# Kernel tuning notes

Measured on AMD Instinct MI355X. Metric: run time of the kernel, lower is better.

## Reference

```python
import jax, jax.numpy as jnp
import numpy as np

ALPHA = 0.2  # LeakyReLU negative slope from init kwarg
NEG_INF = -9e15


def gat_multihead(x, adj_mask, W, a, concat):
    """Standard (GLMP-style) dense GAT, all heads at once.
    x: [B,N,Din], adj_mask: [B,N,N] bool, W: [H,Din,F], a: [H,2F].
    """
    B, N, _ = x.shape
    H, _, F = W.shape
    Wh = jnp.einsum('bnd,hdf->bhnf', x, W)              # [B,H,N,F]
    f1 = jnp.einsum('bhnf,hf->bhn', Wh, a[:, :F])
    f2 = jnp.einsum('bhnf,hf->bhn', Wh, a[:, F:])
    e = jax.nn.leaky_relu(f1[:, :, :, None] + f2[:, :, None, :], ALPHA)  # [B,H,N,N]
    e = jnp.where(adj_mask[:, None], e, NEG_INF)
    att = jax.nn.softmax(e, axis=-1)
    out = jnp.einsum('bhij,bhjf->bhif', att, Wh)        # [B,H,N,F]
    if concat:
        out = jax.nn.elu(out)
        return out.transpose(0, 2, 1, 3).reshape(B, N, H * F)
    # concat=False heads are summed and divided by nheads in load_graph -> mean
    return out.mean(axis=1)


def setup_inputs() -> dict:
    key = jax.random.key(0)
    ks = jax.random.split(key, 12)
    B, N, T = 16, 1024, 6
    V, D, F, H = 32000, 128, 64, 4
    CONV_MAX = 400
    story = jax.random.randint(ks[0], (B, N, T), 0, V)
    kb_len = jax.random.randint(ks[1], (B,), 1, CONV_MAX)
    conv_len = jax.random.randint(ks[2], (B,), 1, CONV_MAX)
    hidden = jax.random.normal(ks[3], (B, F), dtype=jnp.float32)
    dh_outputs = jax.random.normal(ks[4], (B, CONV_MAX, D), dtype=jnp.float32)
    adj = (jax.random.uniform(ks[5], (B, N, N)) < 0.05).astype(jnp.float32)
    emb = jax.random.normal(ks[6], (V, D), dtype=jnp.float32) * 0.1
    W1 = jax.random.normal(ks[7], (H, D, F), dtype=jnp.float32) * 0.1
    a1 = jax.random.normal(ks[8], (H, 2 * F), dtype=jnp.float32) * 0.1
    W2 = jax.random.normal(ks[9], (H, H * F, F), dtype=jnp.float32) * 0.1
    a2 = jax.random.normal(ks[10], (H, 2 * F), dtype=jnp.float32) * 0.1
    W3 = jax.random.normal(ks[11], (H, H * F, F), dtype=jnp.float32) * 0.1
    a3 = jax.random.normal(jax.random.fold_in(key, 99), (H, 2 * F), dtype=jnp.float32) * 0.1
    return {"story": story, "kb_len": kb_len, "conv_len": conv_len,
            "hidden": hidden, "dh_outputs": dh_outputs, "adj": adj,
            "emb": emb, "W1": W1, "a1": a1, "W2": W2, "a2": a2, "W3": W3, "a3": a3}


def reference(story, kb_len, conv_len, hidden, dh_outputs, adj, emb, W1, a1, W2, a2, W3, a3):
    B, N, T = story.shape
    Lc = dh_outputs.shape[1]
    # Embedding lookup + bag-of-words sum over memory token slots
    x = emb[story].sum(axis=2)                              # [B,N,D]
    # add_lm_embedding: scatter dh_outputs[b, :conv_len[b]] into slots
    # [kb_len[b]-1, kb_len[b]-1+conv_len[b]) of the memory (vectorized)
    pos = jnp.arange(N)[None, :]                            # [1,N]
    off = pos - (kb_len[:, None] - 1)                       # [B,N]
    valid = (off >= 0) & (off < conv_len[:, None])
    idx = jnp.clip(off, 0, Lc - 1)
    gathered = jnp.take_along_axis(dh_outputs, idx[:, :, None], axis=1)  # [B,N,D]
    x = x + jnp.where(valid[:, :, None], gathered, 0.0)
    # update_pad_token_adj: self-loop for pad slots k >= kb_len+conv_len
    d = jnp.arange(N)
    start = kb_len + conv_len                               # (kb_len-1)+conv_len+1
    diag = adj[:, d, d]
    adj = adj.at[:, d, d].set(jnp.where(d[None, :] >= start[:, None], 1.0, diag))
    adj_mask = adj > 0
    # Three GAT stacks (dropout omitted: eval mode)
    x = gat_multihead(x, adj_mask, W1, a1, concat=True)     # [B,N,H*F]
    x = gat_multihead(x, adj_mask, W2, a2, concat=True)     # [B,N,H*F]
    x = jax.nn.sigmoid(gat_multihead(x, adj_mask, W3, a3, concat=False))  # [B,N,F]
    prob_logits = jnp.einsum('bnf,bf->bn', x, hidden)       # [B,N]
    return (jax.nn.sigmoid(prob_logits), hidden, prob_logits)
```

## Files before the change

kernel.cpp:

```cpp
#include <hip/hip_runtime.h>
#include <stdint.h>

typedef short bf16x8 __attribute__((ext_vector_type(8)));
typedef float f32x4 __attribute__((ext_vector_type(4)));
typedef unsigned short u16;
typedef unsigned short u16x4 __attribute__((ext_vector_type(4)));
typedef unsigned int u32;
typedef unsigned int u32x4 __attribute__((ext_vector_type(4)));
typedef unsigned long long u64;


__device__ inline u16 f2b(float f) {
    unsigned u = __float_as_uint(f);
    u += 0x7fffu + ((u >> 16) & 1u);
    return (u16)(u >> 16);
}

__device__ inline float wred_sum(float v) {
    #pragma unroll
    for (int m = 32; m >= 1; m >>= 1) v += __shfl_xor(v, m, 64);
    return v;
}

__global__ __launch_bounds__(256) void k_pre(const float* __restrict__ adj,
                                             const int* __restrict__ kb,
                                             const int* __restrict__ cv,
                                             const int* __restrict__ story,
                                             const float* __restrict__ dh,
                                             const float* __restrict__ emb,
                                             u64* __restrict__ mask,
                                             u16* __restrict__ x0) {
    int bid = blockIdx.x;
    int tid = threadIdx.x;
    if (bid < 4096) {
        int w = tid >> 6, l = tid & 63;
        int row = bid * 4 + w;
        int b = row >> 10, i = row & 1023;
        int start = kb[b] + cv[b];
        const float* arow = adj + ((size_t)row << 10);
        u64* mrow = mask + ((size_t)row << 4);
        #pragma unroll
        for (int wd = 0; wd < 16; ++wd) {
            int j = (wd << 6) | l;
            bool p = arow[j] > 0.0f;
            if (j == i && i >= start) p = true;
            u64 bal = __ballot(p);
            if (l == 0) mrow[wd] = bal;
        }
    } else {
        int bn = ((bid - 4096) << 1) + (tid >> 7);
        int b = bn >> 10, n = bn & 1023;
        int d = tid & 127;
        const int* st = story + (size_t)bn * 6;
        float s = 0.0f;
        #pragma unroll
        for (int t = 0; t < 6; ++t) {
            int tok = st[t];
            s += emb[((size_t)tok << 7) + d];
        }
        int off = n - (kb[b] - 1);
        if (off >= 0 && off < cv[b]) s += dh[((size_t)b * 400 + off) * 128 + d];
        x0[((size_t)bn << 7) + d] = f2b(s);
    }
}

__global__ __launch_bounds__(256) void k_wa_all(const float* __restrict__ W1,
                                                const float* __restrict__ a1,
                                                const float* __restrict__ W2,
                                                const float* __restrict__ a2,
                                                const float* __restrict__ W3,
                                                const float* __restrict__ a3,
                                                float* __restrict__ wa) {
    int bid = blockIdx.x;
    const float *W, *a; float* o; int Kmask, kshift;
    if (bid < 4)       { W = W1; a = a1; o = wa;        Kmask = 127; kshift = 7; }
    else if (bid < 12) { W = W2; a = a2; o = wa + 1024; Kmask = 255; kshift = 8; bid -= 4; }
    else               { W = W3; a = a3; o = wa + 3072; Kmask = 255; kshift = 8; bid -= 12; }
    int id = bid * 256 + threadIdx.x;
    int c = id >> kshift, k = id & Kmask;
    int h = c >> 1, wh = c & 1;
    const float4* wr = (const float4*)(W + ((size_t)(h << kshift) + k) * 64);
    const float4* av = (const float4*)(a + h * 128 + wh * 64);
    float s = 0.0f;
    #pragma unroll
    for (int q = 0; q < 16; ++q) {
        float4 x = wr[q], y = av[q];
        s += x.x * y.x + x.y * y.y + x.z * y.z + x.w * y.w;
    }
    o[id] = s;
}

__global__ __launch_bounds__(256) void k_prepW_all(const float* __restrict__ W1,
                                                   const float* __restrict__ W2,
                                                   const float* __restrict__ W3,
                                                   const float* __restrict__ wa,
                                                   u16* __restrict__ Bp1,
                                                   u16* __restrict__ Bp2,
                                                   u16* __restrict__ Bp3) {
    int bid = blockIdx.x;
    const float* W; const float* wav; u16* Bp; int K;
    if (bid < 136)      { W = W1; wav = wa;        Bp = Bp1; K = 128; }
    else if (bid < 408) { W = W2; wav = wa + 1024; Bp = Bp2; K = 256; bid -= 136; }
    else                { W = W3; wav = wa + 3072; Bp = Bp3; K = 256; bid -= 408; }
    int id = bid * 256 + threadIdx.x;
    int j = id & 7, lane = (id >> 3) & 63, fr = id >> 9;
    int kt = fr / 17, ct = fr - kt * 17;
    int kk = (kt << 5) + ((lane >> 4) << 3) + j;
    u16 o;
    if (ct < 16) {
        int col = (ct << 4) | (lane & 15);
        o = f2b(W[((size_t)(col >> 6) * K + kk) * 64 + (col & 63)]);
    } else {
        int c = lane & 15;
        o = (c < 8) ? f2b(wav[c * K + kk]) : (u16)0;
    }
    Bp[id] = o;
}

template <int KT>
__global__ __launch_bounds__(256) void k_gemm(const u16* __restrict__ A,
                                              const u16* __restrict__ Bp,
                                              u16* __restrict__ WhB,
                                              float* __restrict__ f1,
                                              float* __restrict__ f2) {
    constexpr int K = KT * 32;
    __shared__ __align__(16) u16 tile[4][2048];
    int tid = threadIdx.x;
    int w = tid >> 6, l = tid & 63;
    int gw = blockIdx.x * 4 + w;
    int rt = gw >> 1, colhalf = gw & 1;
    int m0 = rt << 4;
    int b = m0 >> 10, n0 = m0 & 1023;
    int jt = n0 >> 5, halfsel = (n0 >> 4) & 1;
    const bf16x8* Av = (const bf16x8*)A;
    const bf16x8* Bv = (const bf16x8*)Bp;
    int arow = m0 + (l & 15);
    bf16x8 af[KT];
    #pragma unroll
    for (int kt = 0; kt < KT; ++kt)
        af[kt] = Av[((size_t)arow * K + (kt << 5) + ((l >> 4) << 3)) >> 3];
    f32x4 acc[8];
    #pragma unroll
    for (int c = 0; c < 8; ++c) acc[c] = f32x4{0.f, 0.f, 0.f, 0.f};
    f32x4 acc16 = {0.f, 0.f, 0.f, 0.f};
    #pragma unroll
    for (int kt = 0; kt < KT; ++kt) {
        #pragma unroll
        for (int c = 0; c < 8; ++c) {
            int ct = (colhalf << 3) + c;
            acc[c] = __builtin_amdgcn_mfma_f32_16x16x32_bf16(
                af[kt], Bv[(kt * 17 + ct) * 64 + l], acc[c], 0, 0, 0);
        }
        if (colhalf == 0)
            acc16 = __builtin_amdgcn_mfma_f32_16x16x32_bf16(
                af[kt], Bv[(kt * 17 + 16) * 64 + l], acc16, 0, 0, 0);
    }
    int co = l & 15, ro = (l >> 4) << 2;
    if (colhalf == 0 && co < 8) {
        int h = co >> 1;
        float* fp = (co & 1) ? f2 : f1;
        int base = (((b << 2) + h) << 10) + n0 + ro;
        #pragma unroll
        for (int r = 0; r < 4; ++r) fp[base + r] = acc16[r];
    }
    u16* tw = tile[w];
    #pragma unroll
    for (int c = 0; c < 8; ++c) {
        int col2 = (c << 4) + co;
        u16x4 pk;
        #pragma unroll
        for (int r = 0; r < 4; ++r) pk[r] = f2b(acc[c][r]);
        *(u16x4*)(tw + (col2 << 4) + ro) = pk;
    }
    __syncthreads();
    int lp = (halfsel << 5) + (l & 31);
    #pragma unroll
    for (int c4 = 0; c4 < 4; ++c4) {
        int combo = (c4 << 1) + (l >> 5);
        int hh = combo >> 2, ft = combo & 3;
        int col2 = (hh << 6) + (ft << 4) + (l & 15);
        int r0 = ((l >> 4) & 1) << 3;
        bf16x8 v = *(const bf16x8*)(tw + (col2 << 4) + r0);
        int h = (colhalf << 1) + hh;
        int bh = (b << 2) + h;
        size_t fidx = (size_t)((bh << 7) + (jt << 2) + ft);
        *(bf16x8*)(WhB + (fidx * 64 + lp) * 8) = v;
    }
}

#define PV_CORE(f2v4, mw, f1i, d0f, fragbase, Bv, acc, accs, g)                  \
    {                                                                            \
        u32 onep = ((l & 15) == 0) ? 0x3F803F80u : 0u;                           \
        u32x4 ov = {onep, onep, onep, onep};                                     \
        bf16x8 sfrag = __builtin_bit_cast(bf16x8, ov);                           \
        for (int jt = 0; jt < 32; ++jt) {                                        \
            u32 sh = mw[jt] >> (g << 3);                                         \
            f32x4 fa = f2v4[(jt << 3) + (g << 1)];                               \
            f32x4 fb = f2v4[(jt << 3) + (g << 1) + 1];                           \
            float p[8];                                                          \
            _Pragma("unroll")                                                    \
            for (int jj = 0; jj < 8; ++jj) {                                     \
                float f2j = (jj < 4) ? fa[jj] : fb[jj - 4];                      \
                float t = f1i + f2j;                                             \
                float e = fmaxf(t, 0.2f * t);                                    \
                float ex;                                                        \
                asm("v_exp_f32 %0, %1" : "=v"(ex) : "v"(e));                     \
                p[jj] = (sh & (1u << jj)) ? ex : d0f;                            \
            }                                                                    \
            u32x4 pk;                                                            \
            _Pragma("unroll")                                                    \
            for (int q = 0; q < 4; ++q) {                                        \
                u32 r;                                                           \
                asm("v_cvt_pk_bf16_f32 %0, %1, %2"                               \
                    : "=v"(r) : "v"(p[2 * q]), "v"(p[2 * q + 1]));               \
                pk[q] = r;                                                       \
            }                                                                    \
            bf16x8 af = __builtin_bit_cast(bf16x8, pk);                          \
            accs = __builtin_amdgcn_mfma_f32_16x16x32_bf16(af, sfrag, accs, 0, 0, 0); \
            _Pragma("unroll")                                                    \
            for (int ft = 0; ft < 4; ++ft)                                       \
                acc[ft] = __builtin_amdgcn_mfma_f32_16x16x32_bf16(               \
                    af, Bv[(size_t)(fragbase + (jt << 2) + ft) * 64 + l], acc[ft], 0, 0, 0); \
        }                                                                        \
    }

__global__ __launch_bounds__(256) void k_pv0(const u32* __restrict__ mask32,
                                             const float* __restrict__ f1g,
                                             const float* __restrict__ f2g,
                                             const bf16x8* __restrict__ Bv,
                                             u16* __restrict__ xout) {
    __shared__ __align__(16) float f2s[1024];
    const float LOG2E = 1.44269504088896340736f;
    int tid = threadIdx.x;
    int w = tid >> 6, l = tid & 63;
    int bh = blockIdx.x >> 4;
    int b = bh >> 2, h = bh & 3;
    int itile = ((blockIdx.x & 15) << 2) + w;
    int i0 = itile << 4;
    for (int idx = tid; idx < 1024; idx += 256) f2s[idx] = f2g[(bh << 10) + idx] * LOG2E;
    __syncthreads();
    int row = l & 15, g = l >> 4;
    int i = i0 + row;
    float f1i = f1g[(bh << 10) + i] * LOG2E;
    const u32x4* m4 = (const u32x4*)(mask32 + (((size_t)(b << 10) + i) << 5));
    u32 mw[32];
    #pragma unroll
    for (int t4 = 0; t4 < 8; ++t4) {
        u32x4 q = m4[t4];
        mw[t4 * 4 + 0] = q[0]; mw[t4 * 4 + 1] = q[1];
        mw[t4 * 4 + 2] = q[2]; mw[t4 * 4 + 3] = q[3];
    }
    u32 anyb = 0;
    #pragma unroll
    for (int jt = 0; jt < 32; ++jt) anyb |= mw[jt];
    float d0f = (anyb == 0u) ? 1.0f : 0.0f;
    f32x4 acc[4];
    #pragma unroll
    for (int ft = 0; ft < 4; ++ft) acc[ft] = f32x4{0.f, 0.f, 0.f, 0.f};
    f32x4 accs = {0.f, 0.f, 0.f, 0.f};
    const f32x4* f2v4 = (const f32x4*)f2s;
    int fragbase = bh << 7;
    PV_CORE(f2v4, mw, f1i, d0f, fragbase, Bv, acc, accs, g)
    #pragma unroll
    for (int reg = 0; reg < 4; ++reg) {
        int orow = (g << 2) + reg;
        float s = __shfl(accs[reg], g << 4, 64);
        float rinv = 1.0f / s;
        int grow = i0 + orow;
        #pragma unroll
        for (int ft = 0; ft < 4; ++ft) {
            float v = acc[ft][reg] * rinv;
            float e2 = v > 0.0f ? v : (__expf(v) - 1.0f);
            xout[((size_t)((b << 10) + grow) << 8) + (h << 6) + (ft << 4) + row] = f2b(e2);
        }
    }
}

__global__ __launch_bounds__(256) void k_pv3(const u32* __restrict__ mask32,
                                             const float* __restrict__ f1g,
                                             const float* __restrict__ f2g,
                                             const bf16x8* __restrict__ Bv,
                                             const float* __restrict__ hidden,
                                             float* __restrict__ dout) {
    __shared__ __align__(16) float shbuf[4096];
    const float LOG2E = 1.44269504088896340736f;
    int tid = threadIdx.x;
    int w = tid >> 6, l = tid & 63;
    int b = blockIdx.x >> 6;
    int itile = blockIdx.x & 63;
    int i0 = itile << 4;
    int bh = (b << 2) + w;
    for (int idx = tid; idx < 4096; idx += 256) shbuf[idx] = f2g[(b << 12) + idx] * LOG2E;
    __syncthreads();
    int row = l & 15, g = l >> 4;
    int i = i0 + row;
    float f1i = f1g[(bh << 10) + i] * LOG2E;
    const u32x4* m4 = (const u32x4*)(mask32 + (((size_t)(b << 10) + i) << 5));
    u32 mw[32];
    #pragma unroll
    for (int t4 = 0; t4 < 8; ++t4) {
        u32x4 q = m4[t4];
        mw[t4 * 4 + 0] = q[0]; mw[t4 * 4 + 1] = q[1];
        mw[t4 * 4 + 2] = q[2]; mw[t4 * 4 + 3] = q[3];
    }
    u32 anyb = 0;
    #pragma unroll
    for (int jt = 0; jt < 32; ++jt) anyb |= mw[jt];
    float d0f = (anyb == 0u) ? 1.0f : 0.0f;
    f32x4 acc[4];
    #pragma unroll
    for (int ft = 0; ft < 4; ++ft) acc[ft] = f32x4{0.f, 0.f, 0.f, 0.f};
    f32x4 accs = {0.f, 0.f, 0.f, 0.f};
    const f32x4* f2v4 = (const f32x4*)(shbuf + (w << 10));
    int fragbase = bh << 7;
    PV_CORE(f2v4, mw, f1i, d0f, fragbase, Bv, acc, accs, g)
    __syncthreads();
    #pragma unroll
    for (int reg = 0; reg < 4; ++reg) {
        int orow = (g << 2) + reg;
        float s = __shfl(accs[reg], g << 4, 64);
        float rinv = 1.0f / s;
        #pragma unroll
        for (int ft = 0; ft < 4; ++ft)
            shbuf[(w << 10) + (orow << 6) + (ft << 4) + row] = acc[ft][reg] * rinv;
    }
    __syncthreads();
    float hid = hidden[(b << 6) + l];
    #pragma unroll
    for (int k = 0; k < 4; ++k) {
        int rl = (k << 2) + w;
        int o = (rl << 6) + l;
        float s = shbuf[o] + shbuf[1024 + o] + shbuf[2048 + o] + shbuf[3072 + o];
        s *= 0.25f;
        float x = 1.0f / (1.0f + __expf(-s));
        float logit = wred_sum(x * hid);
        if (l == 0) {
            int grow = i0 + rl;
            dout[(b << 10) + grow] = 1.0f / (1.0f + __expf(-logit));
            dout[17408 + (b << 10) + grow] = logit;
        }
    }
    if (itile == 0 && w == 0) dout[16384 + (b << 6) + l] = hid;
}

extern "C" void kernel_launch(void* const* d_in, const int* in_sizes, int n_in,
                              void* d_out, int out_size, void* d_ws, size_t ws_size,
                              hipStream_t stream) {
    const int*   story  = (const int*)d_in[0];
    const int*   kb     = (const int*)d_in[1];
    const int*   cv     = (const int*)d_in[2];
    const float* hidden = (const float*)d_in[3];
    const float* dh     = (const float*)d_in[4];
    const float* adj    = (const float*)d_in[5];
    const float* emb    = (const float*)d_in[6];
    const float* W1     = (const float*)d_in[7];
    const float* a1     = (const float*)d_in[8];
    const float* W2     = (const float*)d_in[9];
    const float* a2     = (const float*)d_in[10];
    const float* W3     = (const float*)d_in[11];
    const float* a3     = (const float*)d_in[12];
    float* dout = (float*)d_out;

    char* ws = (char*)d_ws;
    u64*   mask   = (u64*)(ws + 0);
    u32*   mask32 = (u32*)(ws + 0);
    u16*   x0   = (u16*)(ws + 2097152);
    u16*   xbf  = (u16*)(ws + 6291456);
    u16*   WhB  = (u16*)(ws + 14680064);
    float* f1   = (float*)(ws + 23068672);
    float* f2   = (float*)(ws + 23330816);
    u16*   Bp1  = (u16*)(ws + 23592960);
    u16*   Bp2  = (u16*)(ws + 23724032);
    u16*   Bp3  = (u16*)(ws + 23863296);
    float* wa   = (float*)(ws + 24002560);

    k_wa_all<<<20, 256, 0, stream>>>(W1, a1, W2, a2, W3, a3, wa);
    k_prepW_all<<<680, 256, 0, stream>>>(W1, W2, W3, wa, Bp1, Bp2, Bp3);
    k_pre<<<12288, 256, 0, stream>>>(adj, kb, cv, story, dh, emb, mask, x0);

    k_gemm<4><<<512, 256, 0, stream>>>(x0, Bp1, WhB, f1, f2);
    k_pv0<<<1024, 256, 0, stream>>>(mask32, f1, f2, (const bf16x8*)WhB, xbf);

    k_gemm<8><<<512, 256, 0, stream>>>(xbf, Bp2, WhB, f1, f2);
    k_pv0<<<1024, 256, 0, stream>>>(mask32, f1, f2, (const bf16x8*)WhB, xbf);

    k_gemm<8><<<512, 256, 0, stream>>>(xbf, Bp3, WhB, f1, f2);
    k_pv3<<<1024, 256, 0, stream>>>(mask32, f1, f2, (const bf16x8*)WhB, hidden, dout);
}
```

Before: 163.9 us.

## Fuse weight prep into preprocessing and process two row tiles per wave

Merges the weight-projection and weight-packing kernels into the preprocessing kernel, dropping two launches. The mask builder now reads adjacency rows with vectorized loads and also precomputes a per-row empty-mask flag, and the embedding gather switches to float4 accesses. The GEMM and PV kernels each handle two 16-row tiles per wave so B fragments and f2 loads are reused across both. PV now stages mask rows in LDS, which halves the grid size but raises register pressure and lowers occupancy.

```diff
diff --git a/kernel.cpp b/kernel.cpp
--- a/kernel.cpp
+++ b/kernel.cpp
@@ -28,93 +28,102 @@
                                              const int* __restrict__ story,
                                              const float* __restrict__ dh,
                                              const float* __restrict__ emb,
+                                             const float* __restrict__ W1,
+                                             const float* __restrict__ a1,
+                                             const float* __restrict__ W2,
+                                             const float* __restrict__ a2,
+                                             const float* __restrict__ W3,
+                                             const float* __restrict__ a3,
                                              u64* __restrict__ mask,
-                                             u16* __restrict__ x0) {
+                                             u16* __restrict__ x0,
+                                             u16* __restrict__ Bp1,
+                                             u16* __restrict__ Bp2,
+                                             u16* __restrict__ Bp3,
+                                             float* __restrict__ d0g) {
     int bid = blockIdx.x;
     int tid = threadIdx.x;
-    if (bid < 4096) {
+    if (bid < 1024) {
         int w = tid >> 6, l = tid & 63;
-        int row = bid * 4 + w;
-        int b = row >> 10, i = row & 1023;
+        int rbase = (bid << 4) + (w << 2);
+        int b = rbase >> 10;
         int start = kb[b] + cv[b];
-        const float* arow = adj + ((size_t)row << 10);
-        u64* mrow = mask + ((size_t)row << 4);
-        #pragma unroll
-        for (int wd = 0; wd < 16; ++wd) {
-            int j = (wd << 6) | l;
-            bool p = arow[j] > 0.0f;
-            if (j == i && i >= start) p = true;
-            u64 bal = __ballot(p);
-            if (l == 0) mrow[wd] = bal;
-        }
-    } else {
-        int bn = ((bid - 4096) << 1) + (tid >> 7);
+        const float4* a4 = (const float4*)adj;
+        for (int r = 0; r < 4; ++r) {
+            int row = rbase + r;
+            int i = row & 1023;
+            u32 m16 = 0;
+            #pragma unroll
+            for (int q = 0; q < 4; ++q) {
+                float4 v = a4[(size_t)row * 256 + (l << 2) + q];
+                m16 |= (u32)(v.x > 0.0f) << (q * 4);
+                m16 |= (u32)(v.y > 0.0f) << (q * 4 + 1);
+                m16 |= (u32)(v.z > 0.0f) << (q * 4 + 2);
+                m16 |= (u32)(v.w > 0.0f) << (q * 4 + 3);
+            }
+            if (i >= start && (i >> 4) == l) m16 |= 1u << (i & 15);
+            u64 bal = __ballot(m16 != 0);
+            u32 s0 = (u32)__shfl((int)m16, (l << 2) + 0, 64);
+            u32 s1 = (u32)__shfl((int)m16, (l << 2) + 1, 64);
+            u32 s2 = (u32)__shfl((int)m16, (l << 2) + 2, 64);
+            u32 s3 = (u32)__shfl((int)m16, (l << 2) + 3, 64);
+            if (l < 16) {
+                u64 word = (u64)(s0 | (s1 << 16)) | ((u64)(s2 | (s3 << 16)) << 32);
+                mask[((size_t)row << 4) + l] = word;
+            }
+            if (l == 0) d0g[row] = (bal == 0ull) ? 1.0f : 0.0f;
+        }
+    } else if (bid < 3072) {
+        int w = tid >> 6, l = tid & 63;
+        int r = l >> 5, dq = l & 31;
+        int bn = ((bid - 1024) << 3) + (w << 1) + r;
         int b = bn >> 10, n = bn & 1023;
-        int d = tid & 127;
         const int* st = story + (size_t)bn * 6;
-        float s = 0.0f;
+        const float4* emb4 = (const float4*)emb;
+        float4 acc = {0.f, 0.f, 0.f, 0.f};
         #pragma unroll
         for (int t = 0; t < 6; ++t) {
             int tok = st[t];
-            s += emb[((size_t)tok << 7) + d];
+            float4 e = emb4[(size_t)tok * 32 + dq];
+            acc.x += e.x; acc.y += e.y; acc.z += e.z; acc.w += e.w;
         }
         int off = n - (kb[b] - 1);
-        if (off >= 0 && off < cv[b]) s += dh[((size_t)b * 400 + off) * 128 + d];
-        x0[((size_t)bn << 7) + d] = f2b(s);
-    }
-}
-
-__global__ __launch_bounds__(256) void k_wa_all(const float* __restrict__ W1,
-                                                const float* __restrict__ a1,
-                                                const float* __restrict__ W2,
-                                                const float* __restrict__ a2,
-                                                const float* __restrict__ W3,
-                                                const float* __restrict__ a3,
-                                                float* __restrict__ wa) {
-    int bid = blockIdx.x;
-    const float *W, *a; float* o; int Kmask, kshift;
-    if (bid < 4)       { W = W1; a = a1; o = wa;        Kmask = 127; kshift = 7; }
-    else if (bid < 12) { W = W2; a = a2; o = wa + 1024; Kmask = 255; kshift = 8; bid -= 4; }
-    else               { W = W3; a = a3; o = wa + 3072; Kmask = 255; kshift = 8; bid -= 12; }
-    int id = bid * 256 + threadIdx.x;
-    int c = id >> kshift, k = id & Kmask;
-    int h = c >> 1, wh = c & 1;
-    const float4* wr = (const float4*)(W + ((size_t)(h << kshift) + k) * 64);
-    const float4* av = (const float4*)(a + h * 128 + wh * 64);
-    float s = 0.0f;
-    #pragma unroll
-    for (int q = 0; q < 16; ++q) {
-        float4 x = wr[q], y = av[q];
-        s += x.x * y.x + x.y * y.y + x.z * y.z + x.w * y.w;
-    }
-    o[id] = s;
-}
-
-__global__ __launch_bounds__(256) void k_prepW_all(const float* __restrict__ W1,
-                                                   const float* __restrict__ W2,
-                                                   const float* __restrict__ W3,
-                                                   const float* __restrict__ wa,
-                                                   u16* __restrict__ Bp1,
-                                                   u16* __restrict__ Bp2,
-                                                   u16* __restrict__ Bp3) {
-    int bid = blockIdx.x;
-    const float* W; const float* wav; u16* Bp; int K;
-    if (bid < 136)      { W = W1; wav = wa;        Bp = Bp1; K = 128; }
-    else if (bid < 408) { W = W2; wav = wa + 1024; Bp = Bp2; K = 256; bid -= 136; }
-    else                { W = W3; wav = wa + 3072; Bp = Bp3; K = 256; bid -= 408; }
-    int id = bid * 256 + threadIdx.x;
-    int j = id & 7, lane = (id >> 3) & 63, fr = id >> 9;
-    int kt = fr / 17, ct = fr - kt * 17;
-    int kk = (kt << 5) + ((lane >> 4) << 3) + j;
-    u16 o;
-    if (ct < 16) {
-        int col = (ct << 4) | (lane & 15);
-        o = f2b(W[((size_t)(col >> 6) * K + kk) * 64 + (col & 63)]);
+        if (off >= 0 && off < cv[b]) {
+            float4 d = ((const float4*)dh)[((size_t)b * 400 + off) * 32 + dq];
+            acc.x += d.x; acc.y += d.y; acc.z += d.z; acc.w += d.w;
+        }
+        u16x4 pk = {f2b(acc.x), f2b(acc.y), f2b(acc.z), f2b(acc.w)};
+        *(u16x4*)(x0 + ((size_t)bn << 7) + (dq << 2)) = pk;
     } else {
-        int c = lane & 15;
-        o = (c < 8) ? f2b(wav[c * K + kk]) : (u16)0;
-    }
-    Bp[id] = o;
+        int pb = bid - 3072;
+        const float *W, *a; u16* Bp; int K;
+        if (pb < 136)      { W = W1; a = a1; Bp = Bp1; K = 128; }
+        else if (pb < 408) { W = W2; a = a2; Bp = Bp2; K = 256; pb -= 136; }
+        else               { W = W3; a = a3; Bp = Bp3; K = 256; pb -= 408; }
+        int id = pb * 256 + tid;
+        int j = id & 7, lane = (id >> 3) & 63, fr = id >> 9;
+        int kt = fr / 17, ct = fr - kt * 17;
+        int kk = (kt << 5) + ((lane >> 4) << 3) + j;
+        u16 o;
+        if (ct < 16) {
+            int col = (ct << 4) | (lane & 15);
+            o = f2b(W[((size_t)(col >> 6) * K + kk) * 64 + (col & 63)]);
+        } else {
+            int c = lane & 15;
+            if (c < 8) {
+                int h = c >> 1, wh = c & 1;
+                const float4* wr = (const float4*)(W + ((size_t)h * K + kk) * 64);
+                const float4* av = (const float4*)(a + h * 128 + wh * 64);
+                float s = 0.0f;
+                #pragma unroll
+                for (int q = 0; q < 16; ++q) {
+                    float4 x = wr[q], y = av[q];
+                    s += x.x * y.x + x.y * y.y + x.z * y.z + x.w * y.w;
+                }
+                o = f2b(s);
+            } else o = 0;
+        }
+        Bp[id] = o;
+    }
 }
 
 template <int KT>
@@ -124,154 +133,170 @@
                                               float* __restrict__ f1,
                                               float* __restrict__ f2) {
     constexpr int K = KT * 32;
-    __shared__ __align__(16) u16 tile[4][2048];
-    int tid = threadIdx.x;
-    int w = tid >> 6, l = tid & 63;
-    int gw = blockIdx.x * 4 + w;
-    int rt = gw >> 1, colhalf = gw & 1;
-    int m0 = rt << 4;
+    __shared__ __align__(16) u16 tile[4][2][2048];
+    int tid = threadIdx.x, w = tid >> 6, l = tid & 63;
+    int rtp = blockIdx.x;
+    int colq = w;
+    int m0 = rtp << 5;
     int b = m0 >> 10, n0 = m0 & 1023;
-    int jt = n0 >> 5, halfsel = (n0 >> 4) & 1;
+    int jt = n0 >> 5;
     const bf16x8* Av = (const bf16x8*)A;
     const bf16x8* Bv = (const bf16x8*)Bp;
-    int arow = m0 + (l & 15);
-    bf16x8 af[KT];
-    #pragma unroll
-    for (int kt = 0; kt < KT; ++kt)
-        af[kt] = Av[((size_t)arow * K + (kt << 5) + ((l >> 4) << 3)) >> 3];
-    f32x4 acc[8];
-    #pragma unroll
-    for (int c = 0; c < 8; ++c) acc[c] = f32x4{0.f, 0.f, 0.f, 0.f};
-    f32x4 acc16 = {0.f, 0.f, 0.f, 0.f};
+    int arowA = m0 + (l & 15);
+    bf16x8 afA[KT], afB[KT];
     #pragma unroll
     for (int kt = 0; kt < KT; ++kt) {
-        #pragma unroll
-        for (int c = 0; c < 8; ++c) {
-            int ct = (colhalf << 3) + c;
-            acc[c] = __builtin_amdgcn_mfma_f32_16x16x32_bf16(
-                af[kt], Bv[(kt * 17 + ct) * 64 + l], acc[c], 0, 0, 0);
-        }
-        if (colhalf == 0)
-            acc16 = __builtin_amdgcn_mfma_f32_16x16x32_bf16(
-                af[kt], Bv[(kt * 17 + 16) * 64 + l], acc16, 0, 0, 0);
+        size_t base = ((size_t)arowA * K + (kt << 5) + ((l >> 4) << 3)) >> 3;
+        afA[kt] = Av[base];
+        afB[kt] = Av[base + ((16 * K) >> 3)];
+    }
+    f32x4 accA[4], accB[4];
+    #pragma unroll
+    for (int c = 0; c < 4; ++c) { accA[c] = f32x4{0.f,0.f,0.f,0.f}; accB[c] = f32x4{0.f,0.f,0.f,0.f}; }
+    f32x4 acc16A = {0.f,0.f,0.f,0.f}, acc16B = {0.f,0.f,0.f,0.f};
+    #pragma unroll
+    for (int kt = 0; kt < KT; ++kt) {
+        #pragma unroll
+        for (int c = 0; c < 4; ++c) {
+            bf16x8 bv = Bv[(size_t)(kt * 17 + (colq << 2) + c) * 64 + l];
+            accA[c] = __builtin_amdgcn_mfma_f32_16x16x32_bf16(afA[kt], bv, accA[c], 0, 0, 0);
+            accB[c] = __builtin_amdgcn_mfma_f32_16x16x32_bf16(afB[kt], bv, accB[c], 0, 0, 0);
+        }
+        if (colq == 0) {
+            bf16x8 bv = Bv[(size_t)(kt * 17 + 16) * 64 + l];
+            acc16A = __builtin_amdgcn_mfma_f32_16x16x32_bf16(afA[kt], bv, acc16A, 0, 0, 0);
+            acc16B = __builtin_amdgcn_mfma_f32_16x16x32_bf16(afB[kt], bv, acc16B, 0, 0, 0);
+        }
     }
     int co = l & 15, ro = (l >> 4) << 2;
-    if (colhalf == 0 && co < 8) {
-        int h = co >> 1;
+    if (colq == 0 && co < 8) {
+        int hh = co >> 1;
         float* fp = (co & 1) ? f2 : f1;
-        int base = (((b << 2) + h) << 10) + n0 + ro;
-        #pragma unroll
-        for (int r = 0; r < 4; ++r) fp[base + r] = acc16[r];
-    }
-    u16* tw = tile[w];
-    #pragma unroll
-    for (int c = 0; c < 8; ++c) {
+        int base = (((b << 2) + hh) << 10) + n0 + ro;
+        #pragma unroll
+        for (int r = 0; r < 4; ++r) {
+            fp[base + r] = acc16A[r];
+            fp[base + 16 + r] = acc16B[r];
+        }
+    }
+    u16* twA = tile[w][0]; u16* twB = tile[w][1];
+    #pragma unroll
+    for (int c = 0; c < 4; ++c) {
         int col2 = (c << 4) + co;
-        u16x4 pk;
-        #pragma unroll
-        for (int r = 0; r < 4; ++r) pk[r] = f2b(acc[c][r]);
-        *(u16x4*)(tw + (col2 << 4) + ro) = pk;
+        u16x4 pkA, pkB;
+        #pragma unroll
+        for (int r = 0; r < 4; ++r) { pkA[r] = f2b(accA[c][r]); pkB[r] = f2b(accB[c][r]); }
+        *(u16x4*)(twA + (col2 << 4) + ro) = pkA;
+        *(u16x4*)(twB + (col2 << 4) + ro) = pkB;
     }
     __syncthreads();
-    int lp = (halfsel << 5) + (l & 31);
-    #pragma unroll
-    for (int c4 = 0; c4 < 4; ++c4) {
-        int combo = (c4 << 1) + (l >> 5);
-        int hh = combo >> 2, ft = combo & 3;
-        int col2 = (hh << 6) + (ft << 4) + (l & 15);
+    int bh = (b << 2) + colq;
+    int lq = l & 31;
+    #pragma unroll
+    for (int ftq = 0; ftq < 2; ++ftq) {
+        int ft = (ftq << 1) + (l >> 5);
+        int col2 = (ft << 4) + (l & 15);
         int r0 = ((l >> 4) & 1) << 3;
-        bf16x8 v = *(const bf16x8*)(tw + (col2 << 4) + r0);
-        int h = (colhalf << 1) + hh;
-        int bh = (b << 2) + h;
+        bf16x8 vA = *(const bf16x8*)(twA + (col2 << 4) + r0);
+        bf16x8 vB = *(const bf16x8*)(twB + (col2 << 4) + r0);
         size_t fidx = (size_t)((bh << 7) + (jt << 2) + ft);
-        *(bf16x8*)(WhB + (fidx * 64 + lp) * 8) = v;
-    }
-}
-
-#define PV_CORE(f2v4, mw, f1i, d0f, fragbase, Bv, acc, accs, g)                  \
-    {                                                                            \
-        u32 onep = ((l & 15) == 0) ? 0x3F803F80u : 0u;                           \
-        u32x4 ov = {onep, onep, onep, onep};                                     \
-        bf16x8 sfrag = __builtin_bit_cast(bf16x8, ov);                           \
-        for (int jt = 0; jt < 32; ++jt) {                                        \
-            u32 sh = mw[jt] >> (g << 3);                                         \
-            f32x4 fa = f2v4[(jt << 3) + (g << 1)];                               \
-            f32x4 fb = f2v4[(jt << 3) + (g << 1) + 1];                           \
-            float p[8];                                                          \
-            _Pragma("unroll")                                                    \
-            for (int jj = 0; jj < 8; ++jj) {                                     \
-                float f2j = (jj < 4) ? fa[jj] : fb[jj - 4];                      \
-                float t = f1i + f2j;                                             \
-                float e = fmaxf(t, 0.2f * t);                                    \
-                float ex;                                                        \
-                asm("v_exp_f32 %0, %1" : "=v"(ex) : "v"(e));                     \
-                p[jj] = (sh & (1u << jj)) ? ex : d0f;                            \
-            }                                                                    \
-            u32x4 pk;                                                            \
-            _Pragma("unroll")                                                    \
-            for (int q = 0; q < 4; ++q) {                                        \
-                u32 r;                                                           \
-                asm("v_cvt_pk_bf16_f32 %0, %1, %2"                               \
-                    : "=v"(r) : "v"(p[2 * q]), "v"(p[2 * q + 1]));               \
-                pk[q] = r;                                                       \
-            }                                                                    \
-            bf16x8 af = __builtin_bit_cast(bf16x8, pk);                          \
-            accs = __builtin_amdgcn_mfma_f32_16x16x32_bf16(af, sfrag, accs, 0, 0, 0); \
-            _Pragma("unroll")                                                    \
-            for (int ft = 0; ft < 4; ++ft)                                       \
-                acc[ft] = __builtin_amdgcn_mfma_f32_16x16x32_bf16(               \
-                    af, Bv[(size_t)(fragbase + (jt << 2) + ft) * 64 + l], acc[ft], 0, 0, 0); \
-        }                                                                        \
+        *(bf16x8*)(WhB + (fidx * 64 + lq) * 8) = vA;
+        *(bf16x8*)(WhB + (fidx * 64 + 32 + lq) * 8) = vB;
+    }
+}
+
+#define PV_BODY(mrowA, mrowB)                                                      \
+    f32x4 accA[4], accB[4];                                                        \
+    _Pragma("unroll")                                                              \
+    for (int ft = 0; ft < 4; ++ft) { accA[ft] = f32x4{0.f,0.f,0.f,0.f}; accB[ft] = f32x4{0.f,0.f,0.f,0.f}; } \
+    f32x4 accsA = {0.f,0.f,0.f,0.f}, accsB = {0.f,0.f,0.f,0.f};                    \
+    {                                                                              \
+        u32 onep = ((l & 15) == 0) ? 0x3F803F80u : 0u;                             \
+        u32x4 ov = {onep, onep, onep, onep};                                       \
+        bf16x8 sfrag = __builtin_bit_cast(bf16x8, ov);                             \
+        for (int jt = 0; jt < 32; ++jt) {                                          \
+            u32 shA = mrowA[jt] >> (g << 3);                                       \
+            u32 shB = mrowB[jt] >> (g << 3);                                       \
+            f32x4 fa = f2v4[(jt << 3) + (g << 1)];                                 \
+            f32x4 fb = f2v4[(jt << 3) + (g << 1) + 1];                             \
+            float pA[8], pB[8];                                                    \
+            _Pragma("unroll")                                                      \
+            for (int jj = 0; jj < 8; ++jj) {                                       \
+                float f2j = (jj < 4) ? fa[jj] : fb[jj - 4];                        \
+                float tA = f1iA + f2j, tB = f1iB + f2j;                            \
+                float eA = fmaxf(tA, 0.2f * tA), eB = fmaxf(tB, 0.2f * tB);        \
+                float exA, exB;                                                    \
+                asm("v_exp_f32 %0, %1" : "=v"(exA) : "v"(eA));                     \
+                asm("v_exp_f32 %0, %1" : "=v"(exB) : "v"(eB));                     \
+                pA[jj] = (shA & (1u << jj)) ? exA : d0fA;                          \
+                pB[jj] = (shB & (1u << jj)) ? exB : d0fB;                          \
+            }                                                                      \
+            u32x4 pkA, pkB;                                                        \
+            _Pragma("unroll")                                                      \
+            for (int q = 0; q < 4; ++q) {                                          \
+                u32 rA, rB;                                                        \
+                asm("v_cvt_pk_bf16_f32 %0, %1, %2" : "=v"(rA) : "v"(pA[2*q]), "v"(pA[2*q+1])); \
+                asm("v_cvt_pk_bf16_f32 %0, %1, %2" : "=v"(rB) : "v"(pB[2*q]), "v"(pB[2*q+1])); \
+                pkA[q] = rA; pkB[q] = rB;                                          \
+            }                                                                      \
+            bf16x8 afA = __builtin_bit_cast(bf16x8, pkA);                          \
+            bf16x8 afB = __builtin_bit_cast(bf16x8, pkB);                          \
+            accsA = __builtin_amdgcn_mfma_f32_16x16x32_bf16(afA, sfrag, accsA, 0, 0, 0); \
+            accsB = __builtin_amdgcn_mfma_f32_16x16x32_bf16(afB, sfrag, accsB, 0, 0, 0); \
+            _Pragma("unroll")                                                      \
+            for (int ft = 0; ft < 4; ++ft) {                                       \
+                bf16x8 bv = Bv[(size_t)(fragbase + (jt << 2) + ft) * 64 + l];      \
+                accA[ft] = __builtin_amdgcn_mfma_f32_16x16x32_bf16(afA, bv, accA[ft], 0, 0, 0); \
+                accB[ft] = __builtin_amdgcn_mfma_f32_16x16x32_bf16(afB, bv, accB[ft], 0, 0, 0); \
+            }                                                                      \
+        }                                                                          \
     }
 
 __global__ __launch_bounds__(256) void k_pv0(const u32* __restrict__ mask32,
                                              const float* __restrict__ f1g,
                                              const float* __restrict__ f2g,
+                                             const float* __restrict__ d0g,
                                              const bf16x8* __restrict__ Bv,
                                              u16* __restrict__ xout) {
     __shared__ __align__(16) float f2s[1024];
+    __shared__ u32 mlds[128 * 33];
     const float LOG2E = 1.44269504088896340736f;
-    int tid = threadIdx.x;
-    int w = tid >> 6, l = tid & 63;
-    int bh = blockIdx.x >> 4;
+    int tid = threadIdx.x, w = tid >> 6, l = tid & 63;
+    int bh = blockIdx.x >> 3;
     int b = bh >> 2, h = bh & 3;
-    int itile = ((blockIdx.x & 15) << 2) + w;
-    int i0 = itile << 4;
+    int rbase = (blockIdx.x & 7) << 7;
     for (int idx = tid; idx < 1024; idx += 256) f2s[idx] = f2g[(bh << 10) + idx] * LOG2E;
+    const u32* msrc = mask32 + (((size_t)(b << 10) + rbase) << 5);
+    for (int idx = tid; idx < 4096; idx += 256)
+        mlds[(idx >> 5) * 33 + (idx & 31)] = msrc[idx];
     __syncthreads();
     int row = l & 15, g = l >> 4;
-    int i = i0 + row;
-    float f1i = f1g[(bh << 10) + i] * LOG2E;
-    const u32x4* m4 = (const u32x4*)(mask32 + (((size_t)(b << 10) + i) << 5));
-    u32 mw[32];
-    #pragma unroll
-    for (int t4 = 0; t4 < 8; ++t4) {
-        u32x4 q = m4[t4];
-        mw[t4 * 4 + 0] = q[0]; mw[t4 * 4 + 1] = q[1];
-        mw[t4 * 4 + 2] = q[2]; mw[t4 * 4 + 3] = q[3];
-    }
-    u32 anyb = 0;
-    #pragma unroll
-    for (int jt = 0; jt < 32; ++jt) anyb |= mw[jt];
-    float d0f = (anyb == 0u) ? 1.0f : 0.0f;
-    f32x4 acc[4];
-    #pragma unroll
-    for (int ft = 0; ft < 4; ++ft) acc[ft] = f32x4{0.f, 0.f, 0.f, 0.f};
-    f32x4 accs = {0.f, 0.f, 0.f, 0.f};
+    int i0 = rbase + (w << 5);
+    int iA = i0 + row, iB = i0 + 16 + row;
+    float f1iA = f1g[(bh << 10) + iA] * LOG2E;
+    float f1iB = f1g[(bh << 10) + iB] * LOG2E;
+    float d0fA = d0g[(b << 10) + iA];
+    float d0fB = d0g[(b << 10) + iB];
+    const u32* mrowA = mlds + ((w << 5) + row) * 33;
+    const u32* mrowB = mrowA + 16 * 33;
     const f32x4* f2v4 = (const f32x4*)f2s;
     int fragbase = bh << 7;
-    PV_CORE(f2v4, mw, f1i, d0f, fragbase, Bv, acc, accs, g)
+    PV_BODY(mrowA, mrowB)
     #pragma unroll
     for (int reg = 0; reg < 4; ++reg) {
         int orow = (g << 2) + reg;
-        float s = __shfl(accs[reg], g << 4, 64);
-        float rinv = 1.0f / s;
-        int grow = i0 + orow;
+        float sA = __shfl(accsA[reg], g << 4, 64);
+        float sB = __shfl(accsB[reg], g << 4, 64);
+        float rinvA = 1.0f / sA, rinvB = 1.0f / sB;
+        int growA = i0 + orow, growB = i0 + 16 + orow;
         #pragma unroll
         for (int ft = 0; ft < 4; ++ft) {
-            float v = acc[ft][reg] * rinv;
-            float e2 = v > 0.0f ? v : (__expf(v) - 1.0f);
-            xout[((size_t)((b << 10) + grow) << 8) + (h << 6) + (ft << 4) + row] = f2b(e2);
+            float vA = accA[ft][reg] * rinvA;
+            float vB = accB[ft][reg] * rinvB;
+            float eA = vA > 0.0f ? vA : (__expf(vA) - 1.0f);
+            float eB = vB > 0.0f ? vB : (__expf(vB) - 1.0f);
+            xout[((size_t)((b << 10) + growA) << 8) + (h << 6) + (ft << 4) + row] = f2b(eA);
+            xout[((size_t)((b << 10) + growB) << 8) + (h << 6) + (ft << 4) + row] = f2b(eB);
         }
     }
 }
@@ -279,68 +304,64 @@
 __global__ __launch_bounds__(256) void k_pv3(const u32* __restrict__ mask32,
                                              const float* __restrict__ f1g,
                                              const float* __restrict__ f2g,
+                                             const float* __restrict__ d0g,
                                              const bf16x8* __restrict__ Bv,
                                              const float* __restrict__ hidden,
                                              float* __restrict__ dout) {
-    __shared__ __align__(16) float shbuf[4096];
+    __shared__ __align__(16) float shbuf[8192];
+    __shared__ u32 mlds3[32 * 33];
     const float LOG2E = 1.44269504088896340736f;
-    int tid = threadIdx.x;
-    int w = tid >> 6, l = tid & 63;
-    int b = blockIdx.x >> 6;
-    int itile = blockIdx.x & 63;
-    int i0 = itile << 4;
+    int tid = threadIdx.x, w = tid >> 6, l = tid & 63;
+    int b = blockIdx.x >> 5;
+    int itp = blockIdx.x & 31;
+    int i0 = itp << 5;
     int bh = (b << 2) + w;
     for (int idx = tid; idx < 4096; idx += 256) shbuf[idx] = f2g[(b << 12) + idx] * LOG2E;
+    const u32* msrc = mask32 + (((size_t)(b << 10) + i0) << 5);
+    for (int idx = tid; idx < 1024; idx += 256)
+        mlds3[(idx >> 5) * 33 + (idx & 31)] = msrc[idx];
     __syncthreads();
     int row = l & 15, g = l >> 4;
-    int i = i0 + row;
-    float f1i = f1g[(bh << 10) + i] * LOG2E;
-    const u32x4* m4 = (const u32x4*)(mask32 + (((size_t)(b << 10) + i) << 5));
-    u32 mw[32];
-    #pragma unroll
-    for (int t4 = 0; t4 < 8; ++t4) {
-        u32x4 q = m4[t4];
-        mw[t4 * 4 + 0] = q[0]; mw[t4 * 4 + 1] = q[1];
-        mw[t4 * 4 + 2] = q[2]; mw[t4 * 4 + 3] = q[3];
-    }
-    u32 anyb = 0;
-    #pragma unroll
-    for (int jt = 0; jt < 32; ++jt) anyb |= mw[jt];
-    float d0f = (anyb == 0u) ? 1.0f : 0.0f;
-    f32x4 acc[4];
-    #pragma unroll
-    for (int ft = 0; ft < 4; ++ft) acc[ft] = f32x4{0.f, 0.f, 0.f, 0.f};
-    f32x4 accs = {0.f, 0.f, 0.f, 0.f};
+    int iA = i0 + row, iB = i0 + 16 + row;
+    float f1iA = f1g[(bh << 10) + iA] * LOG2E;
+    float f1iB = f1g[(bh << 10) + iB] * LOG2E;
+    float d0fA = d0g[(b << 10) + iA];
+    float d0fB = d0g[(b << 10) + iB];
+    const u32* mrowA = mlds3 + row * 33;
+    const u32* mrowB = mrowA + 16 * 33;
     const f32x4* f2v4 = (const f32x4*)(shbuf + (w << 10));
     int fragbase = bh << 7;
-    PV_CORE(f2v4, mw, f1i, d0f, fragbase, Bv, acc, accs, g)
+    PV_BODY(mrowA, mrowB)
     __syncthreads();
     #pragma unroll
     for (int reg = 0; reg < 4; ++reg) {
         int orow = (g << 2) + reg;
-        float s = __shfl(accs[reg], g << 4, 64);
-        float rinv = 1.0f / s;
-        #pragma unroll
-        for (int ft = 0; ft < 4; ++ft)
-            shbuf[(w << 10) + (orow << 6) + (ft << 4) + row] = acc[ft][reg] * rinv;
+        float sA = __shfl(accsA[reg], g << 4, 64);
+        float sB = __shfl(accsB[reg], g << 4, 64);
+        float rinvA = 1.0f / sA, rinvB = 1.0f / sB;
+        #pragma unroll
+        for (int ft = 0; ft < 4; ++ft) {
+            shbuf[(w << 11) + (orow << 6) + (ft << 4) + row] = accA[ft][reg] * rinvA;
+            shbuf[(w << 11) + ((orow + 16) << 6) + (ft << 4) + row] = accB[ft][reg] * rinvB;
+        }
     }
     __syncthreads();
     float hid = hidden[(b << 6) + l];
     #pragma unroll
-    for (int k = 0; k < 4; ++k) {
-        int rl = (k << 2) + w;
-        int o = (rl << 6) + l;
-        float s = shbuf[o] + shbuf[1024 + o] + shbuf[2048 + o] + shbuf[3072 + o];
+    for (int k = 0; k < 8; ++k) {
+        int r = (k << 2) + w;
+        int o = (r << 6) + l;
+        float s = shbuf[o] + shbuf[2048 + o] + shbuf[4096 + o] + shbuf[6144 + o];
         s *= 0.25f;
         float x = 1.0f / (1.0f + __expf(-s));
         float logit = wred_sum(x * hid);
         if (l == 0) {
-            int grow = i0 + rl;
+            int grow = i0 + r;
             dout[(b << 10) + grow] = 1.0f / (1.0f + __expf(-logit));
             dout[17408 + (b << 10) + grow] = logit;
         }
     }
-    if (itile == 0 && w == 0) dout[16384 + (b << 6) + l] = hid;
+    if (itp == 0 && w == 0) dout[16384 + (b << 6) + l] = hid;
 }
 
 extern "C" void kernel_launch(void* const* d_in, const int* in_sizes, int n_in,
@@ -370,20 +391,20 @@
     float* f1   = (float*)(ws + 23068672);
     float* f2   = (float*)(ws + 23330816);
     u16*   Bp1  = (u16*)(ws + 23592960);
-    u16*   Bp2  = (u16*)(ws + 23724032);
-    u16*   Bp3  = (u16*)(ws + 23863296);
-    float* wa   = (float*)(ws + 24002560);
-
-    k_wa_all<<<20, 256, 0, stream>>>(W1, a1, W2, a2, W3, a3, wa);
-    k_prepW_all<<<680, 256, 0, stream>>>(W1, W2, W3, wa, Bp1, Bp2, Bp3);
-    k_pre<<<12288, 256, 0, stream>>>(adj, kb, cv, story, dh, emb, mask, x0);
+    u16*   Bp2  = (u16*)(ws + 23662592);
+    u16*   Bp3  = (u16*)(ws + 23801856);
+    float* d0g  = (float*)(ws + 23941120);
+
+    k_pre<<<3752, 256, 0, stream>>>(adj, kb, cv, story, dh, emb,
+                                    W1, a1, W2, a2, W3, a3,
+                                    mask, x0, Bp1, Bp2, Bp3, d0g);
 
     k_gemm<4><<<512, 256, 0, stream>>>(x0, Bp1, WhB, f1, f2);
-    k_pv0<<<1024, 256, 0, stream>>>(mask32, f1, f2, (const bf16x8*)WhB, xbf);
+    k_pv0<<<512, 256, 0, stream>>>(mask32, f1, f2, d0g, (const bf16x8*)WhB, xbf);
 
     k_gemm<8><<<512, 256, 0, stream>>>(xbf, Bp2, WhB, f1, f2);
-    k_pv0<<<1024, 256, 0, stream>>>(mask32, f1, f2, (const bf16x8*)WhB, xbf);
+    k_pv0<<<512, 256, 0, stream>>>(mask32, f1, f2, d0g, (const bf16x8*)WhB, xbf);
 
     k_gemm<8><<<512, 256, 0, stream>>>(xbf, Bp3, WhB, f1, f2);
-    k_pv3<<<1024, 256, 0, stream>>>(mask32, f1, f2, (const bf16x8*)WhB, hidden, dout);
-}
+    k_pv3<<<512, 256, 0, stream>>>(mask32, f1, f2, d0g, (const bf16x8*)WhB, hidden, dout);
+}
```

Measured after the change: 210.6 us. 28.5% more time.
